# Kernel tuning notes

Measured on AMD Instinct MI355X. Metric: run time of the kernel, lower is better.

Reference implementation:

```python
import jax, jax.numpy as jnp
import numpy as np

QD, KD, HID, NH = 256, 320, 256, 8
NQ, NK, NB = 4096, 4096, 16
DH = HID // NH
EPS = 1e-5
SCALE = float(1.0 / np.sqrt(DH))


def setup_inputs() -> dict:
    key = jax.random.key(0)
    ks = jax.random.split(key, 12)
    s = 0.02
    return {
        "query_nodes": jax.random.normal(ks[0], (NQ, QD), jnp.float32),
        "key_nodes": jax.random.normal(ks[1], (NK, KD), jnp.float32),
        "Wq": jax.random.normal(ks[2], (QD, HID), jnp.float32) * s,
        "bq": jnp.zeros((HID,), jnp.float32),
        "Wk": jax.random.normal(ks[3], (KD, HID), jnp.float32) * s,
        "bk": jnp.zeros((HID,), jnp.float32),
        "Wv": jax.random.normal(ks[4], (KD, HID), jnp.float32) * s,
        "bv": jnp.zeros((HID,), jnp.float32),
        "in_proj_w": jax.random.normal(ks[5], (3 * HID, HID), jnp.float32) * s,
        "in_proj_b": jnp.zeros((3 * HID,), jnp.float32),
        "mha_ow": jax.random.normal(ks[6], (HID, HID), jnp.float32) * s,
        "mha_ob": jnp.zeros((HID,), jnp.float32),
        "Wo": jax.random.normal(ks[7], (HID, QD), jnp.float32) * s,
        "bo": jnp.zeros((QD,), jnp.float32),
        "ln_g": jnp.ones((QD,), jnp.float32),
        "ln_b": jnp.zeros((QD,), jnp.float32),
        "query_batch_idx": jnp.sort(jax.random.randint(ks[8], (NQ,), 0, NB, jnp.int32)),
        "key_batch_idx": jnp.sort(jax.random.randint(ks[9], (NK,), 0, NB, jnp.int32)),
    }


def reference(query_nodes, key_nodes, Wq, bq, Wk, bk, Wv, bv, in_proj_w, in_proj_b,
              mha_ow, mha_ob, Wo, bo, ln_g, ln_b, query_batch_idx, key_batch_idx):
    # outer projections
    q = query_nodes @ Wq + bq          # [NQ, HID]
    k = key_nodes @ Wk + bk            # [NK, HID]
    v = key_nodes @ Wv + bv            # [NK, HID]
    # nn.MultiheadAttention internal in_proj (weights stored [3H, H], applied as x @ W.T)
    q2 = q @ in_proj_w[:HID].T + in_proj_b[:HID]
    k2 = k @ in_proj_w[HID:2 * HID].T + in_proj_b[HID:2 * HID]
    v2 = v @ in_proj_w[2 * HID:].T + in_proj_b[2 * HID:]
    qh = q2.reshape(NQ, NH, DH)
    kh = k2.reshape(NK, NH, DH)
    vh = v2.reshape(NK, NH, DH)
    scores = jnp.einsum('qhd,khd->hqk', qh, kh) * SCALE   # [NH, NQ, NK]
    mask = query_batch_idx[:, None] != key_batch_idx[None, :]  # True = disallowed
    scores = jnp.where(mask[None], -jnp.inf, scores)
    attn = jax.nn.softmax(scores, axis=-1)
    ctx = jnp.einsum('hqk,khd->qhd', attn, vh).reshape(NQ, HID)
    ctx = ctx @ mha_ow + mha_ob        # MHA internal out_proj
    out = ctx @ Wo + bo                # module out_proj back to query_dim
    x = query_nodes + out              # residual (dropout is identity in eval)
    mu = jnp.mean(x, axis=-1, keepdims=True)
    var = jnp.mean((x - mu) ** 2, axis=-1, keepdims=True)
    return (x - mu) / jnp.sqrt(var + EPS) * ln_g + ln_b
```

## Files before the change

### kernel.cpp

```cpp
#include <hip/hip_runtime.h>
#include <hip/hip_bf16.h>
#include <math.h>

#define NQ 4096
#define NK 4096
#define QD 256
#define KD 320
#define HID 256
#define NH 8
#define DH 32
#define NB 16
#define LN_EPS 1e-5f
#define ATT_SCALE 0.17677669529663687f

typedef unsigned short ushort_t;
typedef __attribute__((ext_vector_type(8))) short bf16x8_t;
typedef __attribute__((ext_vector_type(4))) short bf16x4_t;
typedef __attribute__((ext_vector_type(4))) float f32x4_t;

#define OFF_QNB   0
#define OFF_KNB   524288
#define OFF_Q2B   1179648
#define OFF_K2B   1703936
#define OFF_V2B   2228224
#define OFF_CTXB  2752512
#define OFF_XRES  3276800
#define OFF_WQB   4325376
#define OFF_WKB   4358144
#define OFF_WVB   4399104
#define OFF_WINB  4440064
#define OFF_MOWB  4538368
#define OFF_WOTB  4571136
#define OFF_WQT   4603904
#define OFF_WKT   4636672
#define OFF_WVT   4677632
#define OFF_WOT   4718592
#define OFF_BQ    4751360
#define OFF_BK    4751616
#define OFF_BV    4751872
#define OFF_BINP  4752128
#define OFF_MOB   4752896
#define OFF_BO    4753152
#define OFF_LNG   4753408
#define OFF_LNB   4753664
#define OFF_BEFFQ 4753920
#define OFF_BEFFK 4754176
#define OFF_BEFFV 4754432
#define OFF_BEFFO 4754688
#define OFF_KST   4754944
#define OFF_KEN   4754960
#define OFF_FLAG  4754976

__device__ __forceinline__ float bf16_bits_to_f(ushort_t s) {
    unsigned int u = (unsigned int)s << 16;
    float f;
    __builtin_memcpy(&f, &u, 4);
    return f;
}

__device__ __forceinline__ ushort_t f_to_bf16_bits(float v) {
    __hip_bfloat16 t = (__hip_bfloat16)v;
    ushort_t b;
    __builtin_memcpy(&b, &t, 2);
    return b;
}

__global__ void k_detect(const ushort_t* __restrict__ probe,
                         int* __restrict__ flag) {
    __shared__ float red[4];
    int t = threadIdx.x;
    float mx = 0.f;
    for (int i = t; i < 4096; i += 256) {
        float f = fabsf(bf16_bits_to_f(probe[i]));
        if (!(f == f)) f = 1e38f;
        mx = fmaxf(mx, f);
    }
    for (int off = 32; off; off >>= 1) mx = fmaxf(mx, __shfl_xor(mx, off, 64));
    if ((t & 63) == 0) red[t >> 6] = mx;
    __syncthreads();
    if (t == 0) {
        mx = fmaxf(fmaxf(red[0], red[1]), fmaxf(red[2], red[3]));
        *flag = (mx < 100.f) ? 1 : 0;
    }
}

struct Ptrs16 { const void* p[16]; };

#define CVT_TOTAL 2918912

__global__ void k_cvt_all(Ptrs16 ps, float* __restrict__ ws,
                          const int* __restrict__ flag) {
    const int ns[16]   = {1048576,1310720,65536,256,81920,256,81920,256,
                          196608,768,65536,256,65536,256,256,256};
    const int doff[16] = {OFF_QNB,OFF_KNB,OFF_WQB,OFF_BQ,OFF_WKB,OFF_BK,
                          OFF_WVB,OFF_BV,OFF_WINB,OFF_BINP,OFF_MOWB,
                          OFF_MOB,OFF_WOTB,OFF_BO,OFF_LNG,OFF_LNB};
    const int typ[16]  = {0,0,0,1,0,1,0,1,0,1,0,1,2,1,1,1};
    int gid = blockIdx.x * 256 + threadIdx.x;
    if (gid >= CVT_TOTAL) return;
    int fl = *flag;
    int base = 0;
#pragma unroll
    for (int s = 0; s < 16; ++s) {
        int n = ns[s];
        if (gid < base + n) {
            int i = gid - base;
            if (typ[s] == 1) {
                float v = fl ? bf16_bits_to_f(((const ushort_t*)ps.p[s])[i])
                             : ((const float*)ps.p[s])[i];
                ws[doff[s] + i] = v;
            } else {
                ushort_t h = fl ? ((const ushort_t*)ps.p[s])[i]
                                : f_to_bf16_bits(((const float*)ps.p[s])[i]);
                ushort_t* d = (ushort_t*)(ws + doff[s]);
                int di = (typ[s] == 2) ? ((i & 255) * 256 + (i >> 8)) : i;
                d[di] = h;
            }
            return;
        }
        base += n;
    }
}

__global__ void k_ranges(const int* __restrict__ kb, int* __restrict__ kstart,
                         int* __restrict__ kend) {
    int j = blockIdx.x * 256 + threadIdx.x;
    if (j >= NK) return;
    int b = kb[j];
    if (j == 0) {
        for (int x = 0; x < b; ++x) { kstart[x] = 0; kend[x] = 0; }
        kstart[b] = 0;
    } else {
        int bp = kb[j - 1];
        if (bp != b) {
            kend[bp] = j;
            for (int x = bp + 1; x < b; ++x) { kstart[x] = j; kend[x] = j; }
            kstart[b] = j;
        }
    }
    if (j == NK - 1) {
        kend[b] = NK;
        for (int x = b + 1; x < NB; ++x) { kstart[x] = NK; kend[x] = NK; }
    }
}

template <int K>
__device__ __forceinline__ void mm64(const ushort_t* __restrict__ Xrow,
                                     const ushort_t* __restrict__ Wrow,
                                     f32x4_t acc[4]) {
#pragma unroll
    for (int kc = 0; kc < K; kc += 32) {
        bf16x8_t af = *(const bf16x8_t*)(Xrow + kc);
#pragma unroll
        for (int t = 0; t < 4; ++t) {
            bf16x8_t bfrag = *(const bf16x8_t*)(Wrow + t * 16 * K + kc);
            acc[t] = __builtin_amdgcn_mfma_f32_16x16x32_bf16(af, bfrag, acc[t],
                                                             0, 0, 0);
        }
    }
}

__global__ __launch_bounds__(256) void k_fuse_gemm(
        const ushort_t* __restrict__ winb, const ushort_t* __restrict__ wqb,
        const ushort_t* __restrict__ wkb, const ushort_t* __restrict__ wvb,
        const ushort_t* __restrict__ wotb, const ushort_t* __restrict__ mowb,
        ushort_t* __restrict__ wqt, ushort_t* __restrict__ wkt,
        ushort_t* __restrict__ wvt, ushort_t* __restrict__ wot) {
    int r = blockIdx.x;
    const ushort_t *A, *B;
    ushort_t* Out;
    int N, mb, nb;
    if (r < 16)      { A = winb;          B = wqb;  Out = wqt; N = 256; mb = r >> 2;  nb = r & 3; }
    else if (r < 36) { int rr = r - 16; A = winb + 65536;  B = wkb;  Out = wkt; N = 320; mb = rr / 5; nb = rr % 5; }
    else if (r < 56) { int rr = r - 36; A = winb + 131072; B = wvb;  Out = wvt; N = 320; mb = rr / 5; nb = rr % 5; }
    else             { int rr = r - 56; A = wotb;          B = mowb; Out = wot; N = 256; mb = rr >> 2; nb = rr & 3; }
    int w = threadIdx.x >> 6, lane = threadIdx.x & 63;
    int col = lane & 15, quad = lane >> 4;
    int m0 = mb * 64 + w * 16, n0 = nb * 64;
    f32x4_t acc[4];
#pragma unroll
    for (int t = 0; t < 4; ++t) acc[t] = (f32x4_t){0.f, 0.f, 0.f, 0.f};
    mm64<256>(A + (size_t)(m0 + col) * 256 + quad * 8,
              B + (size_t)(n0 + col) * 256 + quad * 8, acc);
#pragma unroll
    for (int t = 0; t < 4; ++t)
#pragma unroll
        for (int rr = 0; rr < 4; ++rr) {
            int m = m0 + quad * 4 + rr;
            int n = n0 + t * 16 + col;
            Out[(size_t)m * N + n] = f_to_bf16_bits(acc[t][rr]);
        }
}

__global__ void k_bias(const float* __restrict__ bq, const float* __restrict__ bk,
                       const float* __restrict__ bv, const float* __restrict__ binp,
                       const float* __restrict__ mob, const float* __restrict__ bo,
                       const ushort_t* __restrict__ winb,
                       const ushort_t* __restrict__ wotb,
                       float* __restrict__ beffQ, float* __restrict__ beffK,
                       float* __restrict__ beffV, float* __restrict__ beffO) {
    int m = blockIdx.x, j = threadIdx.x;
    float acc = 0.f;
    if (m < 3) {
        const float* b = (m == 0) ? bq : (m == 1) ? bk : bv;
        const ushort_t* wrow = winb + (size_t)(m * 256 + j) * 256;
        for (int k = 0; k < 256; ++k) acc += b[k] * bf16_bits_to_f(wrow[k]);
        acc += binp[m * 256 + j];
        float* o = (m == 0) ? beffQ : (m == 1) ? beffK : beffV;
        o[j] = acc;
    } else {
        const ushort_t* wrow = wotb + (size_t)j * 256;
        for (int k = 0; k < 256; ++k) acc += mob[k] * bf16_bits_to_f(wrow[k]);
        acc += bo[j];
        beffO[j] = acc;
    }
}

template <int K, int OUTBF, int RES>
__global__ __launch_bounds__(256) void k_gemm(
        const ushort_t* __restrict__ X,
        const ushort_t* __restrict__ WT0, const ushort_t* __restrict__ WT1,
        const float* __restrict__ b0, const float* __restrict__ b1,
        void* __restrict__ Z0, void* __restrict__ Z1,
        const ushort_t* __restrict__ res) {
    const ushort_t* WT = blockIdx.z ? WT1 : WT0;
    const float* bias  = blockIdx.z ? b1 : b0;
    void* Z            = blockIdx.z ? Z1 : Z0;
    int w = threadIdx.x >> 6, lane = threadIdx.x & 63;
    int col = lane & 15, quad = lane >> 4;
    int m0 = blockIdx.x * 64 + w * 16, n0 = blockIdx.y * 64;
    f32x4_t acc[4];
#pragma unroll
    for (int t = 0; t < 4; ++t) acc[t] = (f32x4_t){0.f, 0.f, 0.f, 0.f};
    mm64<K>(X + (size_t)(m0 + col) * K + quad * 8,
            WT + (size_t)(n0 + col) * K + quad * 8, acc);
#pragma unroll
    for (int t = 0; t < 4; ++t)
#pragma unroll
        for (int rr = 0; rr < 4; ++rr) {
            int m = m0 + quad * 4 + rr;
            int n = n0 + t * 16 + col;
            float v = acc[t][rr] + bias[n];
            if (RES) v += bf16_bits_to_f(res[(size_t)m * 256 + n]);
            size_t idx = (size_t)m * 256 + n;
            if (OUTBF) ((ushort_t*)Z)[idx] = f_to_bf16_bits(v);
            else       ((float*)Z)[idx] = v;
        }
}

__global__ __launch_bounds__(256) void k_attn_mfma(
        const ushort_t* __restrict__ q2b, const ushort_t* __restrict__ k2b,
        const ushort_t* __restrict__ v2b, const int* __restrict__ qb,
        const int* __restrict__ kst, const int* __restrict__ ken,
        ushort_t* __restrict__ ctxb) {
    int wave = threadIdx.x >> 6;
    int lane = threadIdx.x & 63;
    int qt = blockIdx.x >> 1;
    int h  = ((blockIdx.x & 1) << 2) | wave;
    int q0 = qt * 16;
    int col  = lane & 15;
    int quad = lane >> 4;

    int qq = q0 + col;
    int bq_ = qb[qq];
    int j0q = kst[bq_], j1q = ken[bq_];
    int jlo = j0q, jhi = j1q;
#pragma unroll
    for (int off = 1; off < 16; off <<= 1) {
        jlo = min(jlo, __shfl_xor(jlo, off, 64));
        jhi = max(jhi, __shfl_xor(jhi, off, 64));
    }

    bf16x8_t qf = *(const bf16x8_t*)(q2b + (size_t)qq * HID + h * DH + quad * 8);

    f32x4_t accO = {0.f, 0.f, 0.f, 0.f};
    float m_st = -1e30f, l_st = 0.f;

    for (int kt = jlo; kt < jhi; kt += 16) {
        int krow = kt + col;
        if (krow > NK - 1) krow = NK - 1;
        bf16x8_t kf = *(const bf16x8_t*)(k2b + (size_t)krow * HID + h * DH + quad * 8);
        ushort_t vr[4];
#pragma unroll
        for (int j = 0; j < 4; ++j) {
            int vrow = kt + quad * 4 + j;
            if (vrow > NK - 1) vrow = NK - 1;
            vr[j] = v2b[(size_t)vrow * HID + h * DH + col];
        }
        f32x4_t S = __builtin_amdgcn_mfma_f32_16x16x32_bf16(
            kf, qf, (f32x4_t){0.f, 0.f, 0.f, 0.f}, 0, 0, 0);

        float s[4];
        float mt = -3e38f;
#pragma unroll
        for (int r = 0; r < 4; ++r) {
            int kk = kt + quad * 4 + r;
            bool ok = (kk >= j0q) && (kk < j1q);
            s[r] = ok ? S[r] * ATT_SCALE : -3e38f;
            mt = fmaxf(mt, s[r]);
        }
        mt = fmaxf(mt, __shfl_xor(mt, 16, 64));
        mt = fmaxf(mt, __shfl_xor(mt, 32, 64));
        float m_new = fmaxf(m_st, mt);
        float alpha = __expf(m_st - m_new);
        float p[4], ps = 0.f;
#pragma unroll
        for (int r = 0; r < 4; ++r) { p[r] = __expf(s[r] - m_new); ps += p[r]; }
        ps += __shfl_xor(ps, 16, 64);
        ps += __shfl_xor(ps, 32, 64);
        l_st = l_st * alpha + ps;
        m_st = m_new;

        bf16x4_t pb, vb;
#pragma unroll
        for (int r = 0; r < 4; ++r) {
            pb[r] = (short)f_to_bf16_bits(p[r]);
            vb[r] = (short)vr[r];
        }
#pragma unroll
        for (int r = 0; r < 4; ++r) {
            float aq = __shfl(alpha, quad * 4 + r, 64);
            accO[r] *= aq;
        }
        accO = __builtin_amdgcn_mfma_f32_16x16x16bf16_1k(pb, vb, accO, 0, 0, 0);
    }

#pragma unroll
    for (int r = 0; r < 4; ++r) {
        float lq = __shfl(l_st, quad * 4 + r, 64);
        float o = (lq > 0.f) ? accO[r] / lq : 0.f;
        int qrow = q0 + quad * 4 + r;
        ctxb[(size_t)qrow * HID + h * DH + col] = f_to_bf16_bits(o);
    }
}

__global__ void k_ln(const float* __restrict__ X, const float* __restrict__ g,
                     const float* __restrict__ bb, void* __restrict__ out,
                     const int* __restrict__ flag) {
    __shared__ float red[8];
    int q = blockIdx.x, t = threadIdx.x;
    float x = X[(size_t)q * QD + t];
    float s = x, ss = x * x;
    for (int off = 32; off; off >>= 1) {
        s += __shfl_xor(s, off, 64);
        ss += __shfl_xor(ss, off, 64);
    }
    int w = t >> 6;
    if ((t & 63) == 0) { red[w] = s; red[4 + w] = ss; }
    __syncthreads();
    s = red[0] + red[1] + red[2] + red[3];
    ss = red[4] + red[5] + red[6] + red[7];
    float mu = s * (1.f / QD);
    float var = ss * (1.f / QD) - mu * mu;
    float inv = rsqrtf(var + LN_EPS);
    float y = (x - mu) * inv * g[t] + bb[t];
    size_t idx = (size_t)q * QD + t;
    if (*flag)
        ((__hip_bfloat16*)out)[idx] = (__hip_bfloat16)y;
    else
        ((float*)out)[idx] = y;
}

extern "C" void kernel_launch(void* const* d_in, const int* in_sizes, int n_in,
                              void* d_out, int out_size, void* d_ws, size_t ws_size,
                              hipStream_t stream) {
    const int* qbi = (const int*)d_in[16];
    const int* kbi = (const int*)d_in[17];

    float* w = (float*)d_ws;
    ushort_t* qnb  = (ushort_t*)(w + OFF_QNB);
    ushort_t* knb  = (ushort_t*)(w + OFF_KNB);
    ushort_t* q2b  = (ushort_t*)(w + OFF_Q2B);
    ushort_t* k2b  = (ushort_t*)(w + OFF_K2B);
    ushort_t* v2b  = (ushort_t*)(w + OFF_V2B);
    ushort_t* ctxb = (ushort_t*)(w + OFF_CTXB);
    float*    xres = w + OFF_XRES;
    ushort_t* wqb  = (ushort_t*)(w + OFF_WQB);
    ushort_t* wkb  = (ushort_t*)(w + OFF_WKB);
    ushort_t* wvb  = (ushort_t*)(w + OFF_WVB);
    ushort_t* winb = (ushort_t*)(w + OFF_WINB);
    ushort_t* mowb = (ushort_t*)(w + OFF_MOWB);
    ushort_t* wotb = (ushort_t*)(w + OFF_WOTB);
    ushort_t* wqt  = (ushort_t*)(w + OFF_WQT);
    ushort_t* wkt  = (ushort_t*)(w + OFF_WKT);
    ushort_t* wvt  = (ushort_t*)(w + OFF_WVT);
    ushort_t* wot  = (ushort_t*)(w + OFF_WOT);
    float* beffQ = w + OFF_BEFFQ;
    float* beffK = w + OFF_BEFFK;
    float* beffV = w + OFF_BEFFV;
    float* beffO = w + OFF_BEFFO;
    int* kst  = (int*)(w + OFF_KST);
    int* ken  = (int*)(w + OFF_KEN);
    int* flag = (int*)(w + OFF_FLAG);

    Ptrs16 ps;
    for (int i = 0; i < 16; ++i) ps.p[i] = d_in[i];

    k_detect<<<1, 256, 0, stream>>>((const ushort_t*)d_in[0], flag);
    k_cvt_all<<<(CVT_TOTAL + 255) / 256, 256, 0, stream>>>(ps, w, flag);
    k_ranges<<<NK / 256, 256, 0, stream>>>(kbi, kst, ken);
    k_fuse_gemm<<<72, 256, 0, stream>>>(winb, wqb, wkb, wvb, wotb, mowb,
                                        wqt, wkt, wvt, wot);
    k_bias<<<4, 256, 0, stream>>>(w + OFF_BQ, w + OFF_BK, w + OFF_BV,
                                  w + OFF_BINP, w + OFF_MOB, w + OFF_BO,
                                  winb, wotb, beffQ, beffK, beffV, beffO);
    k_gemm<256, 1, 0><<<dim3(NQ / 64, 4, 1), 256, 0, stream>>>(
        qnb, wqt, wqt, beffQ, beffQ, q2b, q2b, nullptr);
    k_gemm<320, 1, 0><<<dim3(NK / 64, 4, 2), 256, 0, stream>>>(
        knb, wkt, wvt, beffK, beffV, k2b, v2b, nullptr);
    k_attn_mfma<<<(NQ / 16) * 2, 256, 0, stream>>>(q2b, k2b, v2b, qbi, kst, ken,
                                                   ctxb);
    k_gemm<256, 0, 1><<<dim3(NQ / 64, 4, 1), 256, 0, stream>>>(
        ctxb, wot, wot, beffO, beffO, xres, xres, qnb);
    k_ln<<<NQ, 256, 0, stream>>>(xres, w + OFF_LNG, w + OFF_LNB, d_out, flag);
}
```

Before: 170.5 us.

## Fuse all stages into one cooperative persistent kernel with grid syncs

Replaces the chain of nine kernel launches with a single cooperative kernel that runs detection, conversion, weight fusion, projections, attention and the output GEMM with LayerNorm, separated by grid-wide barriers. It also fuses the final GEMM with the residual add and LayerNorm, so the fp32 residual buffer is no longer written and read back, and vectorises the input conversion. The goal is to remove launch gaps and the intermediate round-trips. The cost is that the grid is capped at the occupancy limit, which may leave the attention and projection phases with less parallelism, and every block repeats the detection probe. The old multi-kernel path stays as a fallback if the cooperative launch fails.

```diff
diff --git a/kernel.cpp b/kernel.cpp
--- a/kernel.cpp
+++ b/kernel.cpp
@@ -1,4 +1,5 @@
 #include <hip/hip_runtime.h>
+#include <hip/hip_cooperative_groups.h>
 #include <hip/hip_bf16.h>
 #include <math.h>
 
@@ -17,6 +18,7 @@
 typedef __attribute__((ext_vector_type(8))) short bf16x8_t;
 typedef __attribute__((ext_vector_type(4))) short bf16x4_t;
 typedef __attribute__((ext_vector_type(4))) float f32x4_t;
+typedef __attribute__((ext_vector_type(8))) unsigned short ushortx8_t;
 
 #define OFF_QNB   0
 #define OFF_KNB   524288
@@ -65,6 +67,393 @@
     return b;
 }
 
+template <int K>
+__device__ __forceinline__ void mm64(const ushort_t* __restrict__ Xrow,
+                                     const ushort_t* __restrict__ Wrow,
+                                     f32x4_t acc[4]) {
+#pragma unroll
+    for (int kc = 0; kc < K; kc += 32) {
+        bf16x8_t af = *(const bf16x8_t*)(Xrow + kc);
+#pragma unroll
+        for (int t = 0; t < 4; ++t) {
+            bf16x8_t bfrag = *(const bf16x8_t*)(Wrow + t * 16 * K + kc);
+            acc[t] = __builtin_amdgcn_mfma_f32_16x16x32_bf16(af, bfrag, acc[t],
+                                                             0, 0, 0);
+        }
+    }
+}
+
+struct KArgs {
+    const void* in[18];
+    float* ws;
+    void* out;
+};
+
+__global__ __launch_bounds__(256, 2) void k_mega(KArgs a) {
+    cooperative_groups::grid_group grid = cooperative_groups::this_grid();
+    float* ws = a.ws;
+    const int tid = threadIdx.x, bid = blockIdx.x;
+    const int lane = tid & 63, wv = tid >> 6;
+    const int col = lane & 15, quad = lane >> 4;
+    const int gblocks = gridDim.x;
+    const int gstride = gblocks * 256;
+
+    __shared__ float s_red[4];
+    __shared__ int s_flag;
+
+    {
+        const ushort_t* probe = (const ushort_t*)a.in[0];
+        float mx = 0.f;
+        for (int i = tid; i < 4096; i += 256) {
+            float f = fabsf(bf16_bits_to_f(probe[i]));
+            if (!(f == f)) f = 1e38f;
+            mx = fmaxf(mx, f);
+        }
+        for (int off = 32; off; off >>= 1)
+            mx = fmaxf(mx, __shfl_xor(mx, off, 64));
+        if (lane == 0) s_red[wv] = mx;
+        __syncthreads();
+        if (tid == 0) {
+            float m2 = fmaxf(fmaxf(s_red[0], s_red[1]),
+                             fmaxf(s_red[2], s_red[3]));
+            s_flag = (m2 < 100.f) ? 1 : 0;
+        }
+        __syncthreads();
+    }
+    const int fl = s_flag;
+
+    if (bid < 16) {
+        const int* kb = (const int*)a.in[17];
+        int* kstart = (int*)(ws + OFF_KST);
+        int* kend   = (int*)(ws + OFF_KEN);
+        int j = bid * 256 + tid;
+        if (j < NK) {
+            int b = kb[j];
+            if (j == 0) {
+                for (int x = 0; x < b; ++x) { kstart[x] = 0; kend[x] = 0; }
+                kstart[b] = 0;
+            } else {
+                int bp = kb[j - 1];
+                if (bp != b) {
+                    kend[bp] = j;
+                    for (int x = bp + 1; x < b; ++x) { kstart[x] = j; kend[x] = j; }
+                    kstart[b] = j;
+                }
+            }
+            if (j == NK - 1) {
+                kend[b] = NK;
+                for (int x = b + 1; x < NB; ++x) { kstart[x] = NK; kend[x] = NK; }
+            }
+        }
+    }
+    {
+        const int uend[16] = {131072,294912,303104,303136,313376,313408,323648,
+                              323680,348256,348352,356544,356576,364768,364800,
+                              364832,364864};
+        const int doff[16] = {OFF_QNB,OFF_KNB,OFF_WQB,OFF_BQ,OFF_WKB,OFF_BK,
+                              OFF_WVB,OFF_BV,OFF_WINB,OFF_BINP,OFF_MOWB,
+                              OFF_MOB,OFF_WOTB,OFF_BO,OFF_LNG,OFF_LNB};
+        const int typ[16]  = {0,0,0,1,0,1,0,1,0,1,0,1,2,1,1,1};
+        for (int u = bid * 256 + tid; u < 364864; u += gstride) {
+            int s = 0;
+            while (u >= uend[s]) ++s;
+            int ubase = s ? uend[s - 1] : 0;
+            int i0 = (u - ubase) * 8;
+            const void* src = a.in[s];
+            int ty = typ[s];
+            if (ty == 1) {
+                f32x4_t f0, f1;
+                if (fl) {
+                    ushortx8_t h = *(const ushortx8_t*)((const ushort_t*)src + i0);
+#pragma unroll
+                    for (int e = 0; e < 4; ++e) f0[e] = bf16_bits_to_f(h[e]);
+#pragma unroll
+                    for (int e = 0; e < 4; ++e) f1[e] = bf16_bits_to_f(h[4 + e]);
+                } else {
+                    f0 = *(const f32x4_t*)((const float*)src + i0);
+                    f1 = *(const f32x4_t*)((const float*)src + i0 + 4);
+                }
+                float* d = ws + doff[s] + i0;
+                *(f32x4_t*)d = f0;
+                *(f32x4_t*)(d + 4) = f1;
+            } else {
+                ushort_t h8[8];
+                if (fl) {
+                    ushortx8_t h = *(const ushortx8_t*)((const ushort_t*)src + i0);
+#pragma unroll
+                    for (int e = 0; e < 8; ++e) h8[e] = h[e];
+                } else {
+                    f32x4_t f0 = *(const f32x4_t*)((const float*)src + i0);
+                    f32x4_t f1 = *(const f32x4_t*)((const float*)src + i0 + 4);
+#pragma unroll
+                    for (int e = 0; e < 4; ++e) h8[e] = f_to_bf16_bits(f0[e]);
+#pragma unroll
+                    for (int e = 0; e < 4; ++e) h8[4 + e] = f_to_bf16_bits(f1[e]);
+                }
+                ushort_t* d = (ushort_t*)(ws + doff[s]);
+                if (ty == 0) {
+                    ushortx8_t hv;
+#pragma unroll
+                    for (int e = 0; e < 8; ++e) hv[e] = h8[e];
+                    *(ushortx8_t*)(d + i0) = hv;
+                } else {
+                    int k = i0 >> 8, n0 = i0 & 255;
+#pragma unroll
+                    for (int e = 0; e < 8; ++e) d[(n0 + e) * 256 + k] = h8[e];
+                }
+            }
+        }
+    }
+    grid.sync();
+
+    if (bid < 72) {
+        const ushort_t* winb = (const ushort_t*)(ws + OFF_WINB);
+        const ushort_t *A, *B;
+        ushort_t* Out;
+        int N, mb, nb;
+        int r = bid;
+        if (r < 16)      { A = winb;          B = (const ushort_t*)(ws + OFF_WQB);  Out = (ushort_t*)(ws + OFF_WQT); N = 256; mb = r >> 2;  nb = r & 3; }
+        else if (r < 36) { int rr = r - 16; A = winb + 65536;  B = (const ushort_t*)(ws + OFF_WKB);  Out = (ushort_t*)(ws + OFF_WKT); N = 320; mb = rr / 5; nb = rr % 5; }
+        else if (r < 56) { int rr = r - 36; A = winb + 131072; B = (const ushort_t*)(ws + OFF_WVB);  Out = (ushort_t*)(ws + OFF_WVT); N = 320; mb = rr / 5; nb = rr % 5; }
+        else             { int rr = r - 56; A = (const ushort_t*)(ws + OFF_WOTB); B = (const ushort_t*)(ws + OFF_MOWB); Out = (ushort_t*)(ws + OFF_WOT); N = 256; mb = rr >> 2; nb = rr & 3; }
+        int m0 = mb * 64 + wv * 16, n0 = nb * 64;
+        f32x4_t acc[4];
+#pragma unroll
+        for (int t = 0; t < 4; ++t) acc[t] = (f32x4_t){0.f, 0.f, 0.f, 0.f};
+        mm64<256>(A + (size_t)(m0 + col) * 256 + quad * 8,
+                  B + (size_t)(n0 + col) * 256 + quad * 8, acc);
+#pragma unroll
+        for (int t = 0; t < 4; ++t)
+#pragma unroll
+            for (int rr = 0; rr < 4; ++rr) {
+                int m = m0 + quad * 4 + rr;
+                int n = n0 + t * 16 + col;
+                Out[(size_t)m * N + n] = f_to_bf16_bits(acc[t][rr]);
+            }
+    } else if (bid < 76) {
+        int m = bid - 72, j = tid;
+        const ushort_t* winb = (const ushort_t*)(ws + OFF_WINB);
+        const ushort_t* wotb = (const ushort_t*)(ws + OFF_WOTB);
+        float acc = 0.f;
+        if (m < 3) {
+            const float* b = (m == 0) ? (ws + OFF_BQ) : (m == 1) ? (ws + OFF_BK)
+                                                                 : (ws + OFF_BV);
+            const ushort_t* wrow = winb + (size_t)(m * 256 + j) * 256;
+            for (int k = 0; k < 256; ++k) acc += b[k] * bf16_bits_to_f(wrow[k]);
+            acc += (ws + OFF_BINP)[m * 256 + j];
+            float* o = (m == 0) ? (ws + OFF_BEFFQ) : (m == 1) ? (ws + OFF_BEFFK)
+                                                              : (ws + OFF_BEFFV);
+            o[j] = acc;
+        } else {
+            const float* mob = ws + OFF_MOB;
+            const ushort_t* wrow = wotb + (size_t)j * 256;
+            for (int k = 0; k < 256; ++k) acc += mob[k] * bf16_bits_to_f(wrow[k]);
+            acc += (ws + OFF_BO)[j];
+            (ws + OFF_BEFFO)[j] = acc;
+        }
+    }
+    grid.sync();
+
+    for (int u = bid; u < 768; u += gblocks) {
+        const ushort_t* X;
+        const ushort_t* WT;
+        const float* bias;
+        ushort_t* Z;
+        int mt, nt, KK;
+        if (u < 256) {
+            X = (const ushort_t*)(ws + OFF_QNB); WT = (const ushort_t*)(ws + OFF_WQT);
+            bias = ws + OFF_BEFFQ; Z = (ushort_t*)(ws + OFF_Q2B);
+            mt = u >> 2; nt = u & 3; KK = 256;
+        } else if (u < 512) {
+            int uu = u - 256;
+            X = (const ushort_t*)(ws + OFF_KNB); WT = (const ushort_t*)(ws + OFF_WKT);
+            bias = ws + OFF_BEFFK; Z = (ushort_t*)(ws + OFF_K2B);
+            mt = uu >> 2; nt = uu & 3; KK = 320;
+        } else {
+            int uu = u - 512;
+            X = (const ushort_t*)(ws + OFF_KNB); WT = (const ushort_t*)(ws + OFF_WVT);
+            bias = ws + OFF_BEFFV; Z = (ushort_t*)(ws + OFF_V2B);
+            mt = uu >> 2; nt = uu & 3; KK = 320;
+        }
+        int m0 = mt * 64 + wv * 16, n0 = nt * 64;
+        f32x4_t acc[4];
+#pragma unroll
+        for (int t = 0; t < 4; ++t) acc[t] = (f32x4_t){0.f, 0.f, 0.f, 0.f};
+        if (KK == 256)
+            mm64<256>(X + (size_t)(m0 + col) * 256 + quad * 8,
+                      WT + (size_t)(n0 + col) * 256 + quad * 8, acc);
+        else
+            mm64<320>(X + (size_t)(m0 + col) * 320 + quad * 8,
+                      WT + (size_t)(n0 + col) * 320 + quad * 8, acc);
+#pragma unroll
+        for (int t = 0; t < 4; ++t)
+#pragma unroll
+            for (int rr = 0; rr < 4; ++rr) {
+                int m = m0 + quad * 4 + rr;
+                int n = n0 + t * 16 + col;
+                Z[(size_t)m * 256 + n] = f_to_bf16_bits(acc[t][rr] + bias[n]);
+            }
+    }
+    grid.sync();
+
+    for (int u = bid; u < 512; u += gblocks) {
+        const ushort_t* q2b = (const ushort_t*)(ws + OFF_Q2B);
+        const ushort_t* k2b = (const ushort_t*)(ws + OFF_K2B);
+        const ushort_t* v2b = (const ushort_t*)(ws + OFF_V2B);
+        const int* qb  = (const int*)a.in[16];
+        const int* kst = (const int*)(ws + OFF_KST);
+        const int* ken = (const int*)(ws + OFF_KEN);
+        ushort_t* ctxb = (ushort_t*)(ws + OFF_CTXB);
+
+        int qt = u >> 1;
+        int h  = ((u & 1) << 2) | wv;
+        int q0 = qt * 16;
+
+        int qq = q0 + col;
+        int bq_ = qb[qq];
+        int j0q = kst[bq_], j1q = ken[bq_];
+        int jlo = j0q, jhi = j1q;
+#pragma unroll
+        for (int off = 1; off < 16; off <<= 1) {
+            jlo = min(jlo, __shfl_xor(jlo, off, 64));
+            jhi = max(jhi, __shfl_xor(jhi, off, 64));
+        }
+
+        bf16x8_t qf = *(const bf16x8_t*)(q2b + (size_t)qq * HID + h * DH + quad * 8);
+
+        f32x4_t accO = {0.f, 0.f, 0.f, 0.f};
+        float m_st = -1e30f, l_st = 0.f;
+
+        for (int kt = jlo; kt < jhi; kt += 16) {
+            int krow = kt + col;
+            if (krow > NK - 1) krow = NK - 1;
+            bf16x8_t kf = *(const bf16x8_t*)(k2b + (size_t)krow * HID + h * DH + quad * 8);
+            ushort_t vr[4];
+#pragma unroll
+            for (int j = 0; j < 4; ++j) {
+                int vrow = kt + quad * 4 + j;
+                if (vrow > NK - 1) vrow = NK - 1;
+                vr[j] = v2b[(size_t)vrow * HID + h * DH + col];
+            }
+            f32x4_t S = __builtin_amdgcn_mfma_f32_16x16x32_bf16(
+                kf, qf, (f32x4_t){0.f, 0.f, 0.f, 0.f}, 0, 0, 0);
+
+            float s[4];
+            float mt = -3e38f;
+#pragma unroll
+            for (int r = 0; r < 4; ++r) {
+                int kk = kt + quad * 4 + r;
+                bool ok = (kk >= j0q) && (kk < j1q);
+                s[r] = ok ? S[r] * ATT_SCALE : -3e38f;
+                mt = fmaxf(mt, s[r]);
+            }
+            mt = fmaxf(mt, __shfl_xor(mt, 16, 64));
+            mt = fmaxf(mt, __shfl_xor(mt, 32, 64));
+            float m_new = fmaxf(m_st, mt);
+            float alpha = __expf(m_st - m_new);
+            float p[4], ps = 0.f;
+#pragma unroll
+            for (int r = 0; r < 4; ++r) { p[r] = __expf(s[r] - m_new); ps += p[r]; }
+            ps += __shfl_xor(ps, 16, 64);
+            ps += __shfl_xor(ps, 32, 64);
+            l_st = l_st * alpha + ps;
+            m_st = m_new;
+
+            bf16x4_t pb, vb;
+#pragma unroll
+            for (int r = 0; r < 4; ++r) {
+                pb[r] = (short)f_to_bf16_bits(p[r]);
+                vb[r] = (short)vr[r];
+            }
+#pragma unroll
+            for (int r = 0; r < 4; ++r) {
+                float aq = __shfl(alpha, quad * 4 + r, 64);
+                accO[r] *= aq;
+            }
+            accO = __builtin_amdgcn_mfma_f32_16x16x16bf16_1k(pb, vb, accO, 0, 0, 0);
+        }
+
+#pragma unroll
+        for (int r = 0; r < 4; ++r) {
+            float lq = __shfl(l_st, quad * 4 + r, 64);
+            float o = (lq > 0.f) ? accO[r] / lq : 0.f;
+            int qrow = q0 + quad * 4 + r;
+            ctxb[(size_t)qrow * HID + h * DH + col] = f_to_bf16_bits(o);
+        }
+    }
+    grid.sync();
+
+    for (int u = bid; u < 64; u += gblocks) {
+        const ushort_t* ctxb = (const ushort_t*)(ws + OFF_CTXB);
+        const ushort_t* wot  = (const ushort_t*)(ws + OFF_WOT);
+        const ushort_t* qnb  = (const ushort_t*)(ws + OFF_QNB);
+        const float* beffO = ws + OFF_BEFFO;
+        const float* lng = ws + OFF_LNG;
+        const float* lnb = ws + OFF_LNB;
+
+        int m0 = u * 64 + wv * 16;
+        f32x4_t acc[16];
+#pragma unroll
+        for (int t = 0; t < 16; ++t) acc[t] = (f32x4_t){0.f, 0.f, 0.f, 0.f};
+        const ushort_t* Xrow = ctxb + (size_t)(m0 + col) * 256 + quad * 8;
+        const ushort_t* Wbase = wot + (size_t)col * 256 + quad * 8;
+#pragma unroll
+        for (int kc = 0; kc < 256; kc += 32) {
+            bf16x8_t af = *(const bf16x8_t*)(Xrow + kc);
+#pragma unroll
+            for (int t = 0; t < 16; ++t) {
+                bf16x8_t bfrag = *(const bf16x8_t*)(Wbase + (size_t)t * 16 * 256 + kc);
+                acc[t] = __builtin_amdgcn_mfma_f32_16x16x32_bf16(af, bfrag,
+                                                                 acc[t], 0, 0, 0);
+            }
+        }
+        float s_[4] = {0.f, 0.f, 0.f, 0.f};
+        float ss_[4] = {0.f, 0.f, 0.f, 0.f};
+#pragma unroll
+        for (int t = 0; t < 16; ++t) {
+            int n = t * 16 + col;
+            float b = beffO[n];
+#pragma unroll
+            for (int rr = 0; rr < 4; ++rr) {
+                int m = m0 + quad * 4 + rr;
+                float x = acc[t][rr] + b +
+                          bf16_bits_to_f(qnb[(size_t)m * 256 + n]);
+                acc[t][rr] = x;
+                s_[rr] += x;
+                ss_[rr] += x * x;
+            }
+        }
+#pragma unroll
+        for (int off = 1; off < 16; off <<= 1) {
+#pragma unroll
+            for (int rr = 0; rr < 4; ++rr) {
+                s_[rr]  += __shfl_xor(s_[rr],  off, 16);
+                ss_[rr] += __shfl_xor(ss_[rr], off, 16);
+            }
+        }
+        float mu[4], inv[4];
+#pragma unroll
+        for (int rr = 0; rr < 4; ++rr) {
+            mu[rr] = s_[rr] * (1.f / QD);
+            float var = ss_[rr] * (1.f / QD) - mu[rr] * mu[rr];
+            inv[rr] = rsqrtf(var + LN_EPS);
+        }
+#pragma unroll
+        for (int t = 0; t < 16; ++t) {
+            int n = t * 16 + col;
+            float g = lng[n], bb = lnb[n];
+#pragma unroll
+            for (int rr = 0; rr < 4; ++rr) {
+                int m = m0 + quad * 4 + rr;
+                float y = (acc[t][rr] - mu[rr]) * inv[rr] * g + bb;
+                size_t idx = (size_t)m * 256 + n;
+                if (fl) ((ushort_t*)a.out)[idx] = f_to_bf16_bits(y);
+                else    ((float*)a.out)[idx] = y;
+            }
+        }
+    }
+}
+
 __global__ void k_detect(const ushort_t* __restrict__ probe,
                          int* __restrict__ flag) {
     __shared__ float red[4];
@@ -85,7 +474,6 @@
 }
 
 struct Ptrs16 { const void* p[16]; };
-
 #define CVT_TOTAL 2918912
 
 __global__ void k_cvt_all(Ptrs16 ps, float* __restrict__ ws,
@@ -141,22 +529,6 @@
     if (j == NK - 1) {
         kend[b] = NK;
         for (int x = b + 1; x < NB; ++x) { kstart[x] = NK; kend[x] = NK; }
-    }
-}
-
-template <int K>
-__device__ __forceinline__ void mm64(const ushort_t* __restrict__ Xrow,
-                                     const ushort_t* __restrict__ Wrow,
-                                     f32x4_t acc[4]) {
-#pragma unroll
-    for (int kc = 0; kc < K; kc += 32) {
-        bf16x8_t af = *(const bf16x8_t*)(Xrow + kc);
-#pragma unroll
-        for (int t = 0; t < 4; ++t) {
-            bf16x8_t bfrag = *(const bf16x8_t*)(Wrow + t * 16 * K + kc);
-            acc[t] = __builtin_amdgcn_mfma_f32_16x16x32_bf16(af, bfrag, acc[t],
-                                                             0, 0, 0);
-        }
     }
 }
 
@@ -364,10 +736,30 @@
 extern "C" void kernel_launch(void* const* d_in, const int* in_sizes, int n_in,
                               void* d_out, int out_size, void* d_ws, size_t ws_size,
                               hipStream_t stream) {
+    float* w = (float*)d_ws;
+
+    KArgs a;
+    for (int i = 0; i < 18; ++i) a.in[i] = d_in[i];
+    a.ws = w;
+    a.out = d_out;
+
+    int nb = 0;
+    hipError_t oe = hipOccupancyMaxActiveBlocksPerMultiprocessor(
+        &nb, (const void*)k_mega, 256, 0);
+    int grid = 512;
+    if (oe == hipSuccess && nb > 0) {
+        int maxg = nb * 256;
+        if (maxg < grid) grid = maxg;
+    }
+    if (grid < 76) grid = 76;
+
+    void* params[1] = {&a};
+    hipError_t e = hipLaunchCooperativeKernel((const void*)k_mega, dim3(grid),
+                                              dim3(256), params, 0, stream);
+    if (e == hipSuccess) return;
+
     const int* qbi = (const int*)d_in[16];
     const int* kbi = (const int*)d_in[17];
-
-    float* w = (float*)d_ws;
     ushort_t* qnb  = (ushort_t*)(w + OFF_QNB);
     ushort_t* knb  = (ushort_t*)(w + OFF_KNB);
     ushort_t* q2b  = (ushort_t*)(w + OFF_Q2B);
@@ -385,10 +777,6 @@
     ushort_t* wkt  = (ushort_t*)(w + OFF_WKT);
     ushort_t* wvt  = (ushort_t*)(w + OFF_WVT);
     ushort_t* wot  = (ushort_t*)(w + OFF_WOT);
-    float* beffQ = w + OFF_BEFFQ;
-    float* beffK = w + OFF_BEFFK;
-    float* beffV = w + OFF_BEFFV;
-    float* beffO = w + OFF_BEFFO;
     int* kst  = (int*)(w + OFF_KST);
     int* ken  = (int*)(w + OFF_KEN);
     int* flag = (int*)(w + OFF_FLAG);
@@ -403,14 +791,15 @@
                                         wqt, wkt, wvt, wot);
     k_bias<<<4, 256, 0, stream>>>(w + OFF_BQ, w + OFF_BK, w + OFF_BV,
                                   w + OFF_BINP, w + OFF_MOB, w + OFF_BO,
-                                  winb, wotb, beffQ, beffK, beffV, beffO);
+                                  winb, wotb, w + OFF_BEFFQ, w + OFF_BEFFK,
+                                  w + OFF_BEFFV, w + OFF_BEFFO);
     k_gemm<256, 1, 0><<<dim3(NQ / 64, 4, 1), 256, 0, stream>>>(
-        qnb, wqt, wqt, beffQ, beffQ, q2b, q2b, nullptr);
+        qnb, wqt, wqt, w + OFF_BEFFQ, w + OFF_BEFFQ, q2b, q2b, nullptr);
     k_gemm<320, 1, 0><<<dim3(NK / 64, 4, 2), 256, 0, stream>>>(
-        knb, wkt, wvt, beffK, beffV, k2b, v2b, nullptr);
+        knb, wkt, wvt, w + OFF_BEFFK, w + OFF_BEFFV, k2b, v2b, nullptr);
     k_attn_mfma<<<(NQ / 16) * 2, 256, 0, stream>>>(q2b, k2b, v2b, qbi, kst, ken,
                                                    ctxb);
     k_gemm<256, 0, 1><<<dim3(NQ / 64, 4, 1), 256, 0, stream>>>(
-        ctxb, wot, wot, beffO, beffO, xres, xres, qnb);
+        ctxb, wot, wot, w + OFF_BEFFO, w + OFF_BEFFO, xres, xres, qnb);
     k_ln<<<NQ, 256, 0, stream>>>(xres, w + OFF_LNG, w + OFF_LNB, d_out, flag);
 }
```

New measurement: 358.8 us. 110% more time.
